# Performance work log

Measured on AMD Instinct MI355X. Metric: run time of the kernel, lower is better.

The kernel has to match this reference:

```python
import jax, jax.numpy as jnp
import numpy as np

NUM_HEADS = 12

def setup_inputs() -> dict:
    key = jax.random.key(0)
    k1, k2, k3 = jax.random.split(key, 3)
    B, N, C = 8, 1024, 768
    x = jax.random.normal(k1, (B, N, C), dtype=jnp.float32)
    Wqkv = jax.random.normal(k2, (C, 3 * C), dtype=jnp.float32) * (C ** -0.5)
    bqkv = jnp.zeros((3 * C,), dtype=jnp.float32)
    Wproj = jax.random.normal(k3, (C, C), dtype=jnp.float32) * (C ** -0.5)
    bproj = jnp.zeros((C,), dtype=jnp.float32)
    return {"x": x, "Wqkv": Wqkv, "bqkv": bqkv, "Wproj": Wproj, "bproj": bproj}

def reference(x, Wqkv, bqkv, Wproj, bproj):
    B, N, C = x.shape
    H = NUM_HEADS
    D = C // H
    scale = D ** -0.5
    qkv = x @ Wqkv + bqkv                       # [B,N,3C]
    qkv = qkv.reshape(B, N, 3, H, D)
    q, k, v = qkv[:, :, 0], qkv[:, :, 1], qkv[:, :, 2]  # [B,N,H,D]
    attn = jnp.einsum('bnhd,bmhd->bhnm', q, k) * scale  # [B,H,N,N]
    attn = jax.nn.softmax(attn, axis=-1)
    # dropout is identity in eval mode
    out = jnp.einsum('bhnm,bmhd->bnhd', attn, v).reshape(B, N, C)
    out = out @ Wproj + bproj
    return out
```

## Files before the change

### kernel.cpp

```cpp
#include <hip/hip_runtime.h>
#include <hip/hip_bf16.h>
#include <cstdint>
#include <cstddef>

typedef __bf16 bf16;
typedef __bf16 bf16x8 __attribute__((ext_vector_type(8)));
typedef __bf16 bf16x4 __attribute__((ext_vector_type(4)));
typedef __bf16 bf16x2 __attribute__((ext_vector_type(2)));
typedef float f32x4 __attribute__((ext_vector_type(4)));
typedef float f32x16 __attribute__((ext_vector_type(16)));
typedef unsigned int u32;
typedef u32 u32x4 __attribute__((ext_vector_type(4)));

#define LDS_CAST(p) (__attribute__((address_space(3))) void*)(p)
#define GLB_CAST(p) (const __attribute__((address_space(1))) void*)(p)
#define MFMA16(a, b, c) __builtin_amdgcn_mfma_f32_16x16x32_bf16(a, b, c, 0, 0, 0)
#define MFMA32(a, b, c) __builtin_amdgcn_mfma_f32_32x32x16_bf16(a, b, c, 0, 0, 0)

#if __has_builtin(__builtin_amdgcn_exp2f)
#define EXPF(x) __builtin_amdgcn_exp2f(x)
#define QK_SCALE 0.18033688011112042f
#else
#define EXPF(x) __expf(x)
#define QK_SCALE 0.125f
#endif

static constexpr int BATCH = 8;
static constexpr int NSEQ  = 1024;
static constexpr int CDIM  = 768;
static constexpr int NH    = 12;
static constexpr int HD    = 64;
static constexpr int MTOT  = BATCH * NSEQ;
static constexpr int NC3   = 3 * CDIM;

__device__ inline u32 pkbf(float a, float b) {
    bf16x2 t = { (bf16)a, (bf16)b };
    return __builtin_bit_cast(u32, t);
}

__global__ void cast_kernel(const float* __restrict__ src, bf16* __restrict__ dst, int n4) {
    int i = blockIdx.x * blockDim.x + threadIdx.x;
    if (i < n4) {
        float4 v = ((const float4*)src)[i];
        bf16x4 o = { (bf16)v.x, (bf16)v.y, (bf16)v.z, (bf16)v.w };
        ((bf16x4*)dst)[i] = o;
    }
}

__global__ void tcast_kernel(const float* __restrict__ src, bf16* __restrict__ dst,
                             int K, int N) {
    int k = blockIdx.x * blockDim.x + threadIdx.x;
    int n = blockIdx.y;
    if (k < K) dst[(size_t)n * K + k] = (bf16)src[(size_t)k * N + n];
}

template <int MODE>
__global__ __launch_bounds__(256) void gemm_kernel(
    const bf16* __restrict__ A, const bf16* __restrict__ Bt,
    const float* __restrict__ bias, float* __restrict__ outf,
    bf16* __restrict__ q, bf16* __restrict__ kk, bf16* __restrict__ v,
    int Ndim, int K)
{
    __shared__ alignas(16) bf16 sA[128 * 32];
    __shared__ alignas(16) bf16 sB[128 * 32];
    const int tid  = threadIdx.x;
    const int lane = tid & 63;
    const int wid  = tid >> 6;
    const int quad = lane >> 4;
    const int l16  = lane & 15;
    const int wm   = (wid >> 1) * 64;
    const int wn   = (wid & 1) * 64;
    const int tm   = blockIdx.y * 128;
    const int tn   = blockIdx.x * 128;

    const f32x4 fzero = {0.f, 0.f, 0.f, 0.f};
    f32x4 acc[4][4];
#pragma unroll
    for (int i = 0; i < 4; i++)
#pragma unroll
        for (int j = 0; j < 4; j++) acc[i][j] = fzero;

    const int srow = tid >> 2;
    const int sk8  = (tid & 3) * 8;
    const bf16* gA = A  + (size_t)(tm + srow) * K + sk8;
    const bf16* gB = Bt + (size_t)(tn + srow) * K + sk8;
    const size_t rs64 = (size_t)64 * K;
    bf16* dA0 = sA + wid * 512;
    bf16* dA1 = sA + 2048 + wid * 512;
    bf16* dB0 = sB + wid * 512;
    bf16* dB1 = sB + 2048 + wid * 512;

    for (int k0 = 0; k0 < K; k0 += 32) {
        __syncthreads();
        __builtin_amdgcn_global_load_lds(GLB_CAST(gA + k0),        LDS_CAST(dA0), 16, 0, 0);
        __builtin_amdgcn_global_load_lds(GLB_CAST(gA + rs64 + k0), LDS_CAST(dA1), 16, 0, 0);
        __builtin_amdgcn_global_load_lds(GLB_CAST(gB + k0),        LDS_CAST(dB0), 16, 0, 0);
        __builtin_amdgcn_global_load_lds(GLB_CAST(gB + rs64 + k0), LDS_CAST(dB1), 16, 0, 0);
        __syncthreads();

        bf16x8 af[4], bfr[4];
#pragma unroll
        for (int i = 0; i < 4; i++)
            af[i] = *(const bf16x8*)(sA + (wm + i * 16 + l16) * 32 + quad * 8);
#pragma unroll
        for (int i = 0; i < 4; i++)
            bfr[i] = *(const bf16x8*)(sB + (wn + i * 16 + l16) * 32 + quad * 8);
#pragma unroll
        for (int i = 0; i < 4; i++)
#pragma unroll
            for (int j = 0; j < 4; j++) acc[i][j] = MFMA16(af[i], bfr[j], acc[i][j]);
    }

    if (MODE == 0) {
#pragma unroll
        for (int i = 0; i < 4; i++) {
            int row = tm + wm + i * 16 + quad * 4;
#pragma unroll
            for (int j = 0; j < 4; j++) {
                int col = tn + wn + j * 16 + l16;
                float bv = bias[col];
                float* op = outf + (size_t)row * Ndim + col;
#pragma unroll
                for (int r = 0; r < 4; r++) op[(size_t)r * Ndim] = acc[i][j][r] + bv;
            }
        }
    } else {
#pragma unroll
        for (int i = 0; i < 4; i++) {
            int row = tm + wm + i * 16 + quad * 4;
            int b  = row >> 10;
            int ns = row & 1023;
#pragma unroll
            for (int j = 0; j < 4; j++) {
                int col = tn + wn + j * 16 + l16;
                int t3  = col / 768;
                int rem = col - t3 * 768;
                int h = rem >> 6;
                int d = rem & 63;
                float bv = bias[col];
                if (t3 == 0) {
                    bf16* qp = q + ((size_t)(b * NH + h) * NSEQ + ns) * HD + d;
#pragma unroll
                    for (int r = 0; r < 4; r++)
                        qp[(size_t)r * HD] = (bf16)((acc[i][j][r] + bv) * (float)QK_SCALE);
                } else if (t3 == 1) {
                    bf16* kp = kk + ((size_t)(b * NH + h) * NSEQ + ns) * HD + d;
#pragma unroll
                    for (int r = 0; r < 4; r++) kp[(size_t)r * HD] = (bf16)(acc[i][j][r] + bv);
                } else {
                    bf16x4 pv = { (bf16)(acc[i][j][0] + bv), (bf16)(acc[i][j][1] + bv),
                                  (bf16)(acc[i][j][2] + bv), (bf16)(acc[i][j][3] + bv) };
                    *(bf16x4*)(v + ((size_t)(b * NH + h) * HD + d) * NSEQ + ns) = pv;
                }
            }
        }
    }
}

__global__ __launch_bounds__(256) void attn_kernel(
    const bf16* __restrict__ q, const bf16* __restrict__ k,
    const bf16* __restrict__ v, bf16* __restrict__ o)
{
    __shared__ alignas(16) bf16 sQ[128 * 64];
    __shared__ alignas(16) bf16 sK[2][64 * 64];
    __shared__ alignas(16) bf16 sV[2][64 * 64];
    const int tid  = threadIdx.x;
    const int lane = tid & 63;
    const int w    = tid >> 6;
    const int h    = lane >> 5;
    const int l32  = lane & 31;
    const int qt = blockIdx.x;
    const int bh = blockIdx.y;
    const int b = bh / NH, hh = bh - b * NH;

    const bf16* qb = q + ((size_t)bh * NSEQ + qt * 128) * HD;
    const bf16* kb = k + (size_t)bh * NSEQ * HD;
    const bf16* vb = v + (size_t)bh * HD * NSEQ;

#pragma unroll
    for (int i = 0; i < 4; i++) {
        int slot = w * 256 + i * 64 + lane;
        int r = slot >> 3, cs = slot & 7;
        __builtin_amdgcn_global_load_lds(GLB_CAST(qb + r * HD + ((cs ^ (r & 7)) * 8)),
                                         LDS_CAST(sQ + (w * 256 + i * 64) * 8), 16, 0, 0);
    }
    auto stageKV = [&](int kt, int buf) {
#pragma unroll
        for (int i = 0; i < 2; i++) {
            int slot = w * 128 + i * 64 + lane;
            int r = slot >> 3, cs = slot & 7;
            int cc = (cs ^ (r & 7)) * 8;
            __builtin_amdgcn_global_load_lds(GLB_CAST(kb + (size_t)(kt * 64 + r) * HD + cc),
                                             LDS_CAST(&sK[buf][(w * 128 + i * 64) * 8]), 16, 0, 0);
            __builtin_amdgcn_global_load_lds(GLB_CAST(vb + (size_t)r * NSEQ + kt * 64 + cc),
                                             LDS_CAST(&sV[buf][(w * 128 + i * 64) * 8]), 16, 0, 0);
        }
    };
    stageKV(0, 0);
    __syncthreads();

    bf16x8 qf[4];
    {
        int row = w * 32 + l32, rx = row & 7;
#pragma unroll
        for (int cd = 0; cd < 4; cd++)
            qf[cd] = *(const bf16x8*)(sQ + (row * 8 + ((2 * cd + h) ^ rx)) * 8);
    }

    f32x16 accO[2];
#pragma unroll
    for (int dt = 0; dt < 2; dt++)
#pragma unroll
        for (int i = 0; i < 16; i++) accO[dt][i] = 0.f;
    float m_run = -3e38f, l_run = 0.f;

    for (int kt = 0; kt < 16; kt++) {
        const int cur = kt & 1;
        __syncthreads();
        if (kt < 15) stageKV(kt + 1, 1 - cur);
        const bf16* sKc = sK[cur];
        const bf16* sVc = sV[cur];

        f32x16 accS[2];
#pragma unroll
        for (int kvt = 0; kvt < 2; kvt++)
#pragma unroll
            for (int i = 0; i < 16; i++) accS[kvt][i] = 0.f;
#pragma unroll
        for (int kvt = 0; kvt < 2; kvt++) {
            int row = kvt * 32 + l32, rx = row & 7;
#pragma unroll
            for (int cd = 0; cd < 4; cd++) {
                bf16x8 kf = *(const bf16x8*)(sKc + (row * 8 + ((2 * cd + h) ^ rx)) * 8);
                accS[kvt] = MFMA32(kf, qf[cd], accS[kvt]);
            }
        }

        float tmv[16];
#pragma unroll
        for (int i = 0; i < 16; i++) tmv[i] = fmaxf(accS[0][i], accS[1][i]);
#pragma unroll
        for (int s = 8; s >= 1; s >>= 1)
#pragma unroll
            for (int i = 0; i < s; i++) tmv[i] = fmaxf(tmv[i], tmv[i + s]);
        float tmax = fmaxf(tmv[0], __shfl_xor(tmv[0], 32));
        float mnew = fmaxf(m_run, tmax);
        float alpha = EXPF(m_run - mnew);
        m_run = mnew;

        float tsv[16];
#pragma unroll
        for (int kvt = 0; kvt < 2; kvt++)
#pragma unroll
            for (int i = 0; i < 16; i++) {
                float p = EXPF(accS[kvt][i] - mnew);
                accS[kvt][i] = p;
            }
#pragma unroll
        for (int i = 0; i < 16; i++) tsv[i] = accS[0][i] + accS[1][i];
#pragma unroll
        for (int s = 8; s >= 1; s >>= 1)
#pragma unroll
            for (int i = 0; i < s; i++) tsv[i] += tsv[i + s];
        float rs = tsv[0] + __shfl_xor(tsv[0], 32);
        l_run = l_run * alpha + rs;
#pragma unroll
        for (int dt = 0; dt < 2; dt++)
#pragma unroll
            for (int i = 0; i < 16; i++) accO[dt][i] *= alpha;

        u32 pr[2][4][2];
#pragma unroll
        for (int kvt = 0; kvt < 2; kvt++)
#pragma unroll
            for (int g = 0; g < 4; g++) {
                pr[kvt][g][0] = pkbf(accS[kvt][4 * g + 0], accS[kvt][4 * g + 1]);
                pr[kvt][g][1] = pkbf(accS[kvt][4 * g + 2], accS[kvt][4 * g + 3]);
            }
        bf16x8 pf[4];
#pragma unroll
        for (int c = 0; c < 4; c++) {
            int kvt = c >> 1, c1 = c & 1;
            u32 u00 = pr[kvt][2 * c1][0],     u01 = pr[kvt][2 * c1][1];
            u32 u10 = pr[kvt][2 * c1 + 1][0], u11 = pr[kvt][2 * c1 + 1][1];
            u32 y0 = h ? u10 : u00, y1 = h ? u11 : u01;
            u32 z0 = h ? u00 : u10, z1 = h ? u01 : u11;
            u32 w0 = (u32)__shfl_xor((int)z0, 32);
            u32 w1 = (u32)__shfl_xor((int)z1, 32);
            u32x4 fv = { h ? w0 : y0, h ? w1 : y1, h ? y0 : w0, h ? y1 : w1 };
            pf[c] = __builtin_bit_cast(bf16x8, fv);
        }

#pragma unroll
        for (int dt = 0; dt < 2; dt++) {
            int row = dt * 32 + l32, rx = row & 7;
#pragma unroll
            for (int c = 0; c < 4; c++) {
                bf16x8 vf = *(const bf16x8*)(sVc + (row * 8 + ((2 * c + h) ^ rx)) * 8);
                accO[dt] = MFMA32(vf, pf[c], accO[dt]);
            }
        }
    }

    float inv = 1.f / l_run;
    bf16* ob = o + ((size_t)b * NSEQ + qt * 128 + w * 32 + l32) * CDIM + hh * HD;
#pragma unroll
    for (int dt = 0; dt < 2; dt++)
#pragma unroll
        for (int g = 0; g < 4; g++) {
            bf16x4 t = { (bf16)(accO[dt][4 * g + 0] * inv), (bf16)(accO[dt][4 * g + 1] * inv),
                         (bf16)(accO[dt][4 * g + 2] * inv), (bf16)(accO[dt][4 * g + 3] * inv) };
            *(bf16x4*)(ob + dt * 32 + 8 * g + 4 * h) = t;
        }
}

extern "C" void kernel_launch(void* const* d_in, const int* in_sizes, int n_in,
                              void* d_out, int out_size, void* d_ws, size_t ws_size,
                              hipStream_t stream)
{
    const float* x     = (const float*)d_in[0];
    const float* Wqkv  = (const float*)d_in[1];
    const float* bqkv  = (const float*)d_in[2];
    const float* Wproj = (const float*)d_in[3];
    const float* bproj = (const float*)d_in[4];
    float* out = (float*)d_out;

    char* ws = (char*)d_ws;
    const size_t MC2 = (size_t)MTOT * CDIM * 2;
    bf16* xb     = (bf16*)ws; ws += MC2;
    bf16* wqkvt  = (bf16*)ws; ws += (size_t)NC3 * CDIM * 2;
    bf16* wprojt = (bf16*)ws; ws += (size_t)CDIM * CDIM * 2;
    bf16* qw     = (bf16*)ws; ws += MC2;
    bf16* kw     = (bf16*)ws; ws += MC2;
    bf16* vw     = (bf16*)ws; ws += MC2;
    bf16* ow     = (bf16*)ws; ws += MC2;

    int n4 = MTOT * CDIM / 4;
    cast_kernel<<<dim3((n4 + 255) / 256), dim3(256), 0, stream>>>(x, xb, n4);
    tcast_kernel<<<dim3(3, NC3),  dim3(256), 0, stream>>>(Wqkv,  wqkvt,  CDIM, NC3);
    tcast_kernel<<<dim3(3, CDIM), dim3(256), 0, stream>>>(Wproj, wprojt, CDIM, CDIM);

    gemm_kernel<1><<<dim3(NC3 / 128, MTOT / 128), dim3(256), 0, stream>>>(
        xb, wqkvt, bqkv, nullptr, qw, kw, vw, NC3, CDIM);

    attn_kernel<<<dim3(NSEQ / 128, BATCH * NH), dim3(256), 0, stream>>>(qw, kw, vw, ow);

    gemm_kernel<0><<<dim3(CDIM / 128, MTOT / 128), dim3(256), 0, stream>>>(
        ow, wprojt, bproj, out, nullptr, nullptr, nullptr, CDIM, CDIM);
}
```

Before: 227.5 us.

## Double-buffer GEMM LDS tiles, switch to 32x32 MFMA, smaller proj tiles

Measured after the change: 250.1 us. 9.9% more time.

```diff
diff --git a/kernel.cpp b/kernel.cpp
--- a/kernel.cpp
+++ b/kernel.cpp
@@ -14,7 +14,6 @@
 
 #define LDS_CAST(p) (__attribute__((address_space(3))) void*)(p)
 #define GLB_CAST(p) (const __attribute__((address_space(1))) void*)(p)
-#define MFMA16(a, b, c) __builtin_amdgcn_mfma_f32_16x16x32_bf16(a, b, c, 0, 0, 0)
 #define MFMA32(a, b, c) __builtin_amdgcn_mfma_f32_32x32x16_bf16(a, b, c, 0, 0, 0)
 
 #if __has_builtin(__builtin_amdgcn_exp2f)
@@ -54,103 +53,131 @@
     if (k < K) dst[(size_t)n * K + k] = (bf16)src[(size_t)k * N + n];
 }
 
-template <int MODE>
+template <int MODE, int TM>
 __global__ __launch_bounds__(256) void gemm_kernel(
     const bf16* __restrict__ A, const bf16* __restrict__ Bt,
     const float* __restrict__ bias, float* __restrict__ outf,
     bf16* __restrict__ q, bf16* __restrict__ kk, bf16* __restrict__ v,
     int Ndim, int K)
 {
-    __shared__ alignas(16) bf16 sA[128 * 32];
-    __shared__ alignas(16) bf16 sB[128 * 32];
+    constexpr int TU = (TM == 128) ? 2 : 1;
+    constexpr int AI = TM / 64;
+    __shared__ alignas(16) bf16 sA[2][TM * 32];
+    __shared__ alignas(16) bf16 sB[2][128 * 32];
     const int tid  = threadIdx.x;
     const int lane = tid & 63;
-    const int wid  = tid >> 6;
-    const int quad = lane >> 4;
-    const int l16  = lane & 15;
-    const int wm   = (wid >> 1) * 64;
-    const int wn   = (wid & 1) * 64;
-    const int tm   = blockIdx.y * 128;
+    const int w    = tid >> 6;
+    const int h    = lane >> 5;
+    const int l32  = lane & 31;
+    const int wm   = (TM == 128) ? (w >> 1) * 64 : 0;
+    const int wn   = (TM == 128) ? (w & 1) * 64 : w * 32;
+    const int tm   = blockIdx.y * TM;
     const int tn   = blockIdx.x * 128;
 
-    const f32x4 fzero = {0.f, 0.f, 0.f, 0.f};
-    f32x4 acc[4][4];
-#pragma unroll
-    for (int i = 0; i < 4; i++)
-#pragma unroll
-        for (int j = 0; j < 4; j++) acc[i][j] = fzero;
-
-    const int srow = tid >> 2;
-    const int sk8  = (tid & 3) * 8;
-    const bf16* gA = A  + (size_t)(tm + srow) * K + sk8;
-    const bf16* gB = Bt + (size_t)(tn + srow) * K + sk8;
-    const size_t rs64 = (size_t)64 * K;
-    bf16* dA0 = sA + wid * 512;
-    bf16* dA1 = sA + 2048 + wid * 512;
-    bf16* dB0 = sB + wid * 512;
-    bf16* dB1 = sB + 2048 + wid * 512;
-
-    for (int k0 = 0; k0 < K; k0 += 32) {
+    const bf16* gA = A  + (size_t)tm * K;
+    const bf16* gB = Bt + (size_t)tn * K;
+
+    auto stage = [&](int k0, int buf) {
+#pragma unroll
+        for (int i = 0; i < AI; i++) {
+            int s = (w * AI + i) * 64 + lane;
+            int r = s % TM, c = s / TM;
+            __builtin_amdgcn_global_load_lds(GLB_CAST(gA + (size_t)r * K + k0 + c * 8),
+                LDS_CAST(&sA[buf][(w * AI + i) * 512]), 16, 0, 0);
+        }
+#pragma unroll
+        for (int i = 0; i < 2; i++) {
+            int s = (w * 2 + i) * 64 + lane;
+            int r = s & 127, c = s >> 7;
+            __builtin_amdgcn_global_load_lds(GLB_CAST(gB + (size_t)r * K + k0 + c * 8),
+                LDS_CAST(&sB[buf][(w * 2 + i) * 512]), 16, 0, 0);
+        }
+    };
+
+    f32x16 acc[2][TU];
+#pragma unroll
+    for (int t = 0; t < 2; t++)
+#pragma unroll
+        for (int u = 0; u < TU; u++)
+#pragma unroll
+            for (int i = 0; i < 16; i++) acc[t][u][i] = 0.f;
+
+    const int NK = K / 32;
+    stage(0, 0);
+    for (int kt = 0; kt < NK; kt++) {
+        const int cur = kt & 1;
         __syncthreads();
-        __builtin_amdgcn_global_load_lds(GLB_CAST(gA + k0),        LDS_CAST(dA0), 16, 0, 0);
-        __builtin_amdgcn_global_load_lds(GLB_CAST(gA + rs64 + k0), LDS_CAST(dA1), 16, 0, 0);
-        __builtin_amdgcn_global_load_lds(GLB_CAST(gB + k0),        LDS_CAST(dB0), 16, 0, 0);
-        __builtin_amdgcn_global_load_lds(GLB_CAST(gB + rs64 + k0), LDS_CAST(dB1), 16, 0, 0);
-        __syncthreads();
-
-        bf16x8 af[4], bfr[4];
-#pragma unroll
-        for (int i = 0; i < 4; i++)
-            af[i] = *(const bf16x8*)(sA + (wm + i * 16 + l16) * 32 + quad * 8);
-#pragma unroll
-        for (int i = 0; i < 4; i++)
-            bfr[i] = *(const bf16x8*)(sB + (wn + i * 16 + l16) * 32 + quad * 8);
-#pragma unroll
-        for (int i = 0; i < 4; i++)
-#pragma unroll
-            for (int j = 0; j < 4; j++) acc[i][j] = MFMA16(af[i], bfr[j], acc[i][j]);
+        if (kt + 1 < NK) stage((kt + 1) * 32, cur ^ 1);
+        const bf16* sAc = sA[cur];
+        const bf16* sBc = sB[cur];
+
+        bf16x8 af[2][2], bfr[TU][2];
+#pragma unroll
+        for (int t = 0; t < 2; t++)
+#pragma unroll
+            for (int kc = 0; kc < 2; kc++)
+                af[t][kc] = *(const bf16x8*)(sAc + ((kc * 2 + h) * TM + wm + t * 32 + l32) * 8);
+#pragma unroll
+        for (int u = 0; u < TU; u++)
+#pragma unroll
+            for (int kc = 0; kc < 2; kc++)
+                bfr[u][kc] = *(const bf16x8*)(sBc + ((kc * 2 + h) * 128 + wn + u * 32 + l32) * 8);
+#pragma unroll
+        for (int kc = 0; kc < 2; kc++)
+#pragma unroll
+            for (int t = 0; t < 2; t++)
+#pragma unroll
+                for (int u = 0; u < TU; u++)
+                    acc[t][u] = MFMA32(af[t][kc], bfr[u][kc], acc[t][u]);
     }
 
     if (MODE == 0) {
 #pragma unroll
-        for (int i = 0; i < 4; i++) {
-            int row = tm + wm + i * 16 + quad * 4;
-#pragma unroll
-            for (int j = 0; j < 4; j++) {
-                int col = tn + wn + j * 16 + l16;
+        for (int t = 0; t < 2; t++) {
+            int mrow = tm + wm + t * 32 + 4 * h;
+#pragma unroll
+            for (int u = 0; u < TU; u++) {
+                int col = tn + wn + u * 32 + l32;
                 float bv = bias[col];
-                float* op = outf + (size_t)row * Ndim + col;
-#pragma unroll
-                for (int r = 0; r < 4; r++) op[(size_t)r * Ndim] = acc[i][j][r] + bv;
+                float* op = outf + (size_t)mrow * Ndim + col;
+#pragma unroll
+                for (int r = 0; r < 16; r++) {
+                    int rl = (r & 3) + 8 * (r >> 2);
+                    op[(size_t)rl * Ndim] = acc[t][u][r] + bv;
+                }
             }
         }
     } else {
-#pragma unroll
-        for (int i = 0; i < 4; i++) {
-            int row = tm + wm + i * 16 + quad * 4;
-            int b  = row >> 10;
-            int ns = row & 1023;
-#pragma unroll
-            for (int j = 0; j < 4; j++) {
-                int col = tn + wn + j * 16 + l16;
-                int t3  = col / 768;
-                int rem = col - t3 * 768;
-                int h = rem >> 6;
-                int d = rem & 63;
-                float bv = bias[col];
-                if (t3 == 0) {
-                    bf16* qp = q + ((size_t)(b * NH + h) * NSEQ + ns) * HD + d;
-#pragma unroll
-                    for (int r = 0; r < 4; r++)
-                        qp[(size_t)r * HD] = (bf16)((acc[i][j][r] + bv) * (float)QK_SCALE);
-                } else if (t3 == 1) {
-                    bf16* kp = kk + ((size_t)(b * NH + h) * NSEQ + ns) * HD + d;
-#pragma unroll
-                    for (int r = 0; r < 4; r++) kp[(size_t)r * HD] = (bf16)(acc[i][j][r] + bv);
+        const int region = tn / 768;
+        const int rem0 = tn - region * 768 + wn;
+#pragma unroll
+        for (int t = 0; t < 2; t++) {
+            int mrow = tm + wm + t * 32 + 4 * h;
+            int b   = mrow >> 10;
+            int nsb = mrow & 1023;
+#pragma unroll
+            for (int u = 0; u < TU; u++) {
+                int rem = rem0 + u * 32 + l32;
+                int hd = rem >> 6, d = rem & 63;
+                float bv = bias[region * 768 + rem];
+                if (region == 2) {
+                    bf16* vp = v + ((size_t)(b * NH + hd) * HD + d) * NSEQ + nsb;
+#pragma unroll
+                    for (int g = 0; g < 4; g++) {
+                        bf16x4 t4 = { (bf16)(acc[t][u][4 * g + 0] + bv),
+                                      (bf16)(acc[t][u][4 * g + 1] + bv),
+                                      (bf16)(acc[t][u][4 * g + 2] + bv),
+                                      (bf16)(acc[t][u][4 * g + 3] + bv) };
+                        *(bf16x4*)(vp + 8 * g) = t4;
+                    }
                 } else {
-                    bf16x4 pv = { (bf16)(acc[i][j][0] + bv), (bf16)(acc[i][j][1] + bv),
-                                  (bf16)(acc[i][j][2] + bv), (bf16)(acc[i][j][3] + bv) };
-                    *(bf16x4*)(v + ((size_t)(b * NH + h) * HD + d) * NSEQ + ns) = pv;
+                    bf16* qp = (region == 0 ? q : kk) + ((size_t)(b * NH + hd) * NSEQ + nsb) * HD + d;
+                    const float sc = (region == 0) ? (float)QK_SCALE : 1.0f;
+#pragma unroll
+                    for (int r = 0; r < 16; r++) {
+                        int rl = (r & 3) + 8 * (r >> 2);
+                        qp[(size_t)rl * HD] = (bf16)((acc[t][u][r] + bv) * sc);
+                    }
                 }
             }
         }
@@ -340,11 +367,11 @@
     tcast_kernel<<<dim3(3, NC3),  dim3(256), 0, stream>>>(Wqkv,  wqkvt,  CDIM, NC3);
     tcast_kernel<<<dim3(3, CDIM), dim3(256), 0, stream>>>(Wproj, wprojt, CDIM, CDIM);
 
-    gemm_kernel<1><<<dim3(NC3 / 128, MTOT / 128), dim3(256), 0, stream>>>(
+    gemm_kernel<1, 128><<<dim3(NC3 / 128, MTOT / 128), dim3(256), 0, stream>>>(
         xb, wqkvt, bqkv, nullptr, qw, kw, vw, NC3, CDIM);
 
     attn_kernel<<<dim3(NSEQ / 128, BATCH * NH), dim3(256), 0, stream>>>(qw, kw, vw, ow);
 
-    gemm_kernel<0><<<dim3(CDIM / 128, MTOT / 128), dim3(256), 0, stream>>>(
+    gemm_kernel<0, 64><<<dim3(CDIM / 128, MTOT / 64), dim3(256), 0, stream>>>(
         ow, wprojt, bproj, out, nullptr, nullptr, nullptr, CDIM, CDIM);
 }
```
